# Optimization experiments

Measured on AMD Instinct MI355X. Metric: run time of the kernel, lower is better.

The kernel has to match this reference:

```python
import jax, jax.numpy as jnp
import numpy as np

TAU = 2.0      # LIF membrane time constant (spikingjelly default-style, decay_input=True)
VTH = 0.5      # v_threshold from init
S = 4          # time_steps
EPS = 1e-5     # BatchNorm eps
ALPHA = 4.0    # surrogate sigmoid alpha (spikingjelly Sigmoid default)

@jax.custom_vjp
def spike(x):
    # Heaviside forward (spikingjelly: x >= 0 -> 1)
    return (x >= 0.0).astype(x.dtype)

def _spike_fwd(x):
    return spike(x), x

def _spike_bwd(x, g):
    sg = jax.nn.sigmoid(ALPHA * x)
    return (g * ALPHA * sg * (1.0 - sg),)

spike.defvjp(_spike_fwd, _spike_bwd)

def bn(y, gamma, beta, mean, var):
    # inference-mode BatchNorm2d over channel axis 1; y: (B, C, T, V)
    inv = gamma * jax.lax.rsqrt(var + EPS)
    return y * inv[None, :, None, None] + (beta - mean * inv)[None, :, None, None]


def setup_inputs() -> dict:
    key = jax.random.key(0)
    ks = jax.random.split(key, 16)
    B, T, C, V, H, NC = 16, 512, 3, 16, 128, 12
    inp = {
        "x": jax.random.normal(ks[0], (B, T, C, V), dtype=jnp.float32),
        "w1": jax.random.normal(ks[1], (H, C), dtype=jnp.float32) * (1.0 / np.sqrt(C)),
        "b1": jax.random.normal(ks[2], (H,), dtype=jnp.float32) * 0.01,
        "g1": jnp.ones((H,), jnp.float32),
        "be1": jnp.zeros((H,), jnp.float32),
        "m1": jax.random.normal(ks[3], (H,), dtype=jnp.float32) * 0.1,
        "rv1": jax.random.uniform(ks[4], (H,), dtype=jnp.float32) + 0.5,
        "w2": jax.random.normal(ks[5], (H, H), dtype=jnp.float32) * (1.0 / np.sqrt(H)),
        "b2": jax.random.normal(ks[6], (H,), dtype=jnp.float32) * 0.01,
        "g2": jnp.ones((H,), jnp.float32),
        "be2": jnp.zeros((H,), jnp.float32),
        "m2": jax.random.normal(ks[7], (H,), dtype=jnp.float32) * 0.1,
        "rv2": jax.random.uniform(ks[8], (H,), dtype=jnp.float32) + 0.5,
        "wc": jax.random.normal(ks[9], (NC, H), dtype=jnp.float32) * (1.0 / np.sqrt(H)),
        "bc": jax.random.normal(ks[10], (NC,), dtype=jnp.float32) * 0.01,
    }
    return inp


def reference(x, w1, b1, g1, be1, m1, rv1, w2, b2, g2, be2, m2, rv2, wc, bc):
    # x: (B, T, C, V) -> channels-first (B, C, T, V) as in torch permute
    xc = jnp.transpose(x, (0, 2, 1, 3))
    # fc1 1x1 conv + BN; input identical across all S steps, so compute once
    h1 = bn(jnp.einsum('bctv,oc->botv', xc, w1) + b1[None, :, None, None],
            g1, be1, m1, rv1)  # (B, H, T, V)

    def step(carry, _):
        v1s, v2s, acc = carry
        # LIF1: decay_input=True, v_reset=0 hard reset
        v1n = v1s + (h1 - v1s) / TAU
        s1 = spike(v1n - VTH)
        v1n = v1n * (1.0 - s1)
        # fc2 1x1 conv + BN on spikes
        h2 = bn(jnp.einsum('botv,po->bptv', s1, w2) + b2[None, :, None, None],
                g2, be2, m2, rv2)
        # LIF2
        v2n = v2s + (h2 - v2s) / TAU
        s2 = spike(v2n - VTH)
        v2n = v2n * (1.0 - s2)
        return (v1n, v2n, acc + s2), None

    z = jnp.zeros_like(h1)
    (_, _, acc), _ = jax.lax.scan(step, (z, z, z), None, length=S)
    # mean over S, then mean over T and V -> (B, H); dropout is identity in eval
    feat = (acc / S).mean(axis=(2, 3))
    return feat @ wc.T + bc
```

## Files before the change

kernel.cpp:

```cpp
#include <hip/hip_runtime.h>
#include <hip/hip_bf16.h>
#include <stdint.h>
#include <math.h>

#define B_ 16
#define T_ 512
#define V_ 16
#define H_ 128
#define NC_ 12

typedef float v2f __attribute__((ext_vector_type(2)));
typedef __attribute__((ext_vector_type(8))) short s8frag;
typedef __attribute__((ext_vector_type(16))) float f16frag;
typedef unsigned long long u64;


__device__ __forceinline__ unsigned short bf16_rne(float w) {
    unsigned u = __float_as_uint(w);
    unsigned r = (u + 0x7FFFu + ((u >> 16) & 1u)) >> 16;
    return (unsigned short)r;
}
__device__ __forceinline__ float bf16_f32(unsigned short h) {
    return __uint_as_float((unsigned)h << 16);
}
__device__ __forceinline__ void split8(const float* __restrict__ s, s8frag& hi, s8frag& lo) {
    #pragma unroll
    for (int j = 0; j < 8; ++j) {
        float w = s[j];
        unsigned short hb = bf16_rne(w);
        unsigned short lb = bf16_rne(w - bf16_f32(hb));
        hi[j] = (short)hb;
        lo[j] = (short)lb;
    }
}
__device__ __forceinline__ uint4 expand8(unsigned bt) {
    uint4 r;
    r.x = ((bt      & 1u) * 0x3F80u) | (((bt >> 1) & 1u) * 0x3F800000u);
    r.y = (((bt >> 2) & 1u) * 0x3F80u) | (((bt >> 3) & 1u) * 0x3F800000u);
    r.z = (((bt >> 4) & 1u) * 0x3F80u) | (((bt >> 5) & 1u) * 0x3F800000u);
    r.w = (((bt >> 6) & 1u) * 0x3F80u) | (((bt >> 7) & 1u) * 0x3F800000u);
    return r;
}

#define ROUNDS 8
__global__ __launch_bounds__(256, 3) void snn_main(
    const float* __restrict__ x,
    const float* __restrict__ w1, const float* __restrict__ b1,
    const float* __restrict__ g1, const float* __restrict__ be1,
    const float* __restrict__ m1, const float* __restrict__ rv1,
    const float* __restrict__ w2, const float* __restrict__ b2,
    const float* __restrict__ g2, const float* __restrict__ be2,
    const float* __restrict__ m2, const float* __restrict__ rv2,
    float* __restrict__ feat)
{
    __shared__ uint4 afrag[2][2][8][64];
    __shared__ uint4 msk[4][16];
    __shared__ float xs[8 * 3 * V_];

    const int tid  = threadIdx.x;
    const int lane = tid & 63;
    const int wv   = tid >> 6;
    const int nl   = lane & 15;
    const int kg   = (lane >> 4) & 1;
    const int ch4  = lane >> 5;
    const int bb   = blockIdx.x >> 6;
    const int sbase = (blockIdx.x & 63) * (ROUNDS * 16);

    if (tid < 96) {
        const float4* xb = (const float4*)(x + ((size_t)(bb * T_ + (sbase >> 4)) * 3) * V_);
        ((float4*)xs)[tid] = xb[tid];
    }

    const int p = lane, q = lane + 64;
    v2f w0v = { w1[p*3+0], w1[q*3+0] };
    v2f w1v = { w1[p*3+1], w1[q*3+1] };
    v2f w2v = { w1[p*3+2], w1[q*3+2] };
    v2f b1v = { b1[p], b1[q] };
    float i1a = g1[p] * (float)(1.0 / sqrt((double)(rv1[p] + 1e-5f)));
    float i1b = g1[q] * (float)(1.0 / sqrt((double)(rv1[q] + 1e-5f)));
    v2f i1v = { i1a, i1b };
    v2f d1v = { be1[p] - m1[p] * i1a, be1[q] - m1[q] * i1b };

    const int chn = wv * 32 + (lane & 31);
    float i2c = g2[chn] * (float)(1.0 / sqrt((double)(rv2[chn] + 1e-5f)));
    float d2c = be2[chn] - m2[chn] * i2c;
    float b2c = b2[chn];

    s8frag bh[8], bl[8];
    #pragma unroll
    for (int c = 0; c < 8; ++c)
        split8(&w2[chn * H_ + c * 16 + ch4 * 8], bh[c], bl[c]);

    __syncthreads();

    float facc = 0.f;

    #define CONSUME(BUF)                                                        \
        {                                                                       \
            f16frag acc0 = {0.f,0.f,0.f,0.f,0.f,0.f,0.f,0.f,                    \
                            0.f,0.f,0.f,0.f,0.f,0.f,0.f,0.f};                   \
            f16frag acc1 = acc0;                                                \
            _Pragma("unroll")                                                   \
            for (int c = 0; c < 8; ++c) {                                       \
                s8frag a0 = *(const s8frag*)&afrag[BUF][0][c][lane];            \
                s8frag a1 = *(const s8frag*)&afrag[BUF][1][c][lane];            \
                acc0 = __builtin_amdgcn_mfma_f32_32x32x16_bf16(a0, bh[c], acc0, 0,0,0); \
                acc1 = __builtin_amdgcn_mfma_f32_32x32x16_bf16(a1, bh[c], acc1, 0,0,0); \
                acc0 = __builtin_amdgcn_mfma_f32_32x32x16_bf16(a0, bl[c], acc0, 0,0,0); \
                acc1 = __builtin_amdgcn_mfma_f32_32x32x16_bf16(a1, bl[c], acc1, 0,0,0); \
            }                                                                   \
            _Pragma("unroll")                                                   \
            for (int tt = 0; tt < 2; ++tt) {                                    \
                const f16frag accs = tt ? acc1 : acc0;                          \
                _Pragma("unroll")                                               \
                for (int g = 0; g < 4; ++g) {                                   \
                    float v = 0.f;                                              \
                    _Pragma("unroll")                                           \
                    for (int s = 0; s < 4; ++s) {                               \
                        float h2 = (accs[g*4+s] + b2c) * i2c + d2c;             \
                        v = v + (h2 - v) * 0.5f;                                \
                        bool sp = v >= 0.5f;                                    \
                        v = sp ? 0.f : v;                                       \
                        facc += sp ? 1.f : 0.f;                                 \
                    }                                                           \
                }                                                               \
            }                                                                   \
        }

    for (int r = 0; r < ROUNDS; ++r) {
        #pragma unroll
        for (int i = 0; i < 4; ++i) {
            int ls = r * 16 + wv * 4 + i;
            int tl = ls >> 4, v = ls & 15;
            const float* xp = &xs[tl * 48 + v];
            float x0 = xp[0], x1 = xp[V_], x2 = xp[2 * V_];

            v2f h1 = ((x0 * w0v + x1 * w1v + x2 * w2v) + b1v) * i1v + d1v;
            v2f v1t = h1 * 0.5f;
            v2f v2t = v1t + h1 * 0.25f;
            v2f v3t = v2t + (h1 - v2t) * 0.5f;
            v2f v4t = v3t + (h1 - v3t) * 0.5f;

            u64 t1a = __ballot(v1t.x >= 0.5f), t2a = __ballot(v2t.x >= 0.5f);
            u64 t3a = __ballot(v3t.x >= 0.5f), t4a = __ballot(v4t.x >= 0.5f);
            u64 t1b = __ballot(v1t.y >= 0.5f), t2b = __ballot(v2t.y >= 0.5f);
            u64 t3b = __ballot(v3t.y >= 0.5f), t4b = __ballot(v4t.y >= 0.5f);
            u64 s3a = t1a | (t3a & ~t2a), s3b = t1b | (t3b & ~t2b);
            u64 s4a = t2a | (t4a & ~t3a), s4b = t2b | (t4b & ~t3b);

            u64 mx = (lane == 0) ? t1a : (lane == 1) ? t2a : (lane == 2) ? s3a : s4a;
            u64 my = (lane == 0) ? t1b : (lane == 1) ? t2b : (lane == 2) ? s3b : s4b;
            if (lane < 4) {
                uint4 mm;
                mm.x = (unsigned)mx; mm.y = (unsigned)(mx >> 32);
                mm.z = (unsigned)my; mm.w = (unsigned)(my >> 32);
                msk[wv][i * 4 + lane] = mm;
            }
        }
        {
            uint4 mm = msk[wv][nl];
            u64 wsel = ch4 ? ((u64)mm.z | ((u64)mm.w << 32))
                           : ((u64)mm.x | ((u64)mm.y << 32));
            int tt   = wv >> 1;
            int slot = ((wv & 1) * 16 + nl) + 32 * kg;
            int buf  = r & 1;
            #pragma unroll
            for (int j = 0; j < 4; ++j) {
                unsigned by = (unsigned)(wsel >> (kg * 8 + j * 16)) & 0xFFu;
                afrag[buf][tt][ch4 * 4 + j][slot] = expand8(by);
            }
        }
        if (r > 0) { int pb = (r - 1) & 1; CONSUME(pb); }
        __syncthreads();
    }
    { int pb = (ROUNDS - 1) & 1; CONSUME(pb); }
    #undef CONSUME

    facc += __shfl_xor(facc, 32);
    if (lane < 32) atomicAdd(&feat[bb * H_ + chn], facc);
}

__global__ __launch_bounds__(128) void classifier_kernel(
    const float* __restrict__ feat,
    const float* __restrict__ wc,
    const float* __restrict__ bc,
    float* __restrict__ out) {
    __shared__ float fb[H_];
    int b = blockIdx.x, t = threadIdx.x;
    fb[t] = feat[b * H_ + t] * (1.0f / 32768.0f);
    __syncthreads();
    if (t < NC_) {
        float s = 0.f;
        for (int h = 0; h < H_; ++h) s += fb[h] * wc[t * H_ + h];
        out[b * NC_ + t] = s + bc[t];
    }
}

extern "C" void kernel_launch(void* const* d_in, const int* in_sizes, int n_in,
                              void* d_out, int out_size, void* d_ws, size_t ws_size,
                              hipStream_t stream) {
    const float* x   = (const float*)d_in[0];
    const float* w1  = (const float*)d_in[1];
    const float* b1  = (const float*)d_in[2];
    const float* g1  = (const float*)d_in[3];
    const float* be1 = (const float*)d_in[4];
    const float* m1  = (const float*)d_in[5];
    const float* rv1 = (const float*)d_in[6];
    const float* m2  = (const float*)d_in[11];
    const float* w2  = (const float*)d_in[7];
    const float* b2  = (const float*)d_in[8];
    const float* g2  = (const float*)d_in[9];
    const float* be2 = (const float*)d_in[10];
    const float* rv2 = (const float*)d_in[12];
    const float* wc  = (const float*)d_in[13];
    const float* bc  = (const float*)d_in[14];

    float* feat = (float*)d_ws;
    float* out  = (float*)d_out;

    snn_main<<<1024, 256, 0, stream>>>(x, w1, b1, g1, be1, m1, rv1,
                                       w2, b2, g2, be2, m2, rv2, feat);
    classifier_kernel<<<B_, 128, 0, stream>>>(feat, wc, bc, out);
}
```

Measured before the change: 137.3 us.

## Halve rounds per block, drop double buffer, raise occupancy and MFMA priority

Each block now handles half as many rounds, so the grid doubles, and the launch-bound occupancy hint goes from 3 to 6 blocks per CU. The double-buffered afrag staging becomes a single buffer. The software pipeline, where the MFMA for the previous round overlapped with building spikes for the current one, is replaced by a straight sequence: build, sync, MFMA under raised s_setprio, sync, then LIF2. The bias is folded into one fmaf. The intent is to hide latency through more resident waves rather than intra-block pipelining, at the cost of an extra barrier per round and more per-block setup, including the w2 bf16 split repeated by twice as many blocks.

```diff
diff --git a/kernel.cpp b/kernel.cpp
--- a/kernel.cpp
+++ b/kernel.cpp
@@ -42,8 +42,8 @@
     return r;
 }
 
-#define ROUNDS 8
-__global__ __launch_bounds__(256, 3) void snn_main(
+#define ROUNDS 4
+__global__ __launch_bounds__(256, 6) void snn_main(
     const float* __restrict__ x,
     const float* __restrict__ w1, const float* __restrict__ b1,
     const float* __restrict__ g1, const float* __restrict__ be1,
@@ -53,9 +53,9 @@
     const float* __restrict__ m2, const float* __restrict__ rv2,
     float* __restrict__ feat)
 {
-    __shared__ uint4 afrag[2][2][8][64];
+    __shared__ uint4 afrag[2][8][64];
     __shared__ uint4 msk[4][16];
-    __shared__ float xs[8 * 3 * V_];
+    __shared__ float xs[ROUNDS * 2 * 3 * V_];
 
     const int tid  = threadIdx.x;
     const int lane = tid & 63;
@@ -63,10 +63,10 @@
     const int nl   = lane & 15;
     const int kg   = (lane >> 4) & 1;
     const int ch4  = lane >> 5;
-    const int bb   = blockIdx.x >> 6;
-    const int sbase = (blockIdx.x & 63) * (ROUNDS * 16);
-
-    if (tid < 96) {
+    const int bb   = blockIdx.x >> 7;
+    const int sbase = (blockIdx.x & 127) * (ROUNDS * 16);
+
+    if (tid < 48) {
         const float4* xb = (const float4*)(x + ((size_t)(bb * T_ + (sbase >> 4)) * 3) * V_);
         ((float4*)xs)[tid] = xb[tid];
     }
@@ -84,7 +84,7 @@
     const int chn = wv * 32 + (lane & 31);
     float i2c = g2[chn] * (float)(1.0 / sqrt((double)(rv2[chn] + 1e-5f)));
     float d2c = be2[chn] - m2[chn] * i2c;
-    float b2c = b2[chn];
+    float dd2 = fmaf(b2[chn], i2c, d2c);
 
     s8frag bh[8], bl[8];
     #pragma unroll
@@ -94,38 +94,7 @@
     __syncthreads();
 
     float facc = 0.f;
-
-    #define CONSUME(BUF)                                                        \
-        {                                                                       \
-            f16frag acc0 = {0.f,0.f,0.f,0.f,0.f,0.f,0.f,0.f,                    \
-                            0.f,0.f,0.f,0.f,0.f,0.f,0.f,0.f};                   \
-            f16frag acc1 = acc0;                                                \
-            _Pragma("unroll")                                                   \
-            for (int c = 0; c < 8; ++c) {                                       \
-                s8frag a0 = *(const s8frag*)&afrag[BUF][0][c][lane];            \
-                s8frag a1 = *(const s8frag*)&afrag[BUF][1][c][lane];            \
-                acc0 = __builtin_amdgcn_mfma_f32_32x32x16_bf16(a0, bh[c], acc0, 0,0,0); \
-                acc1 = __builtin_amdgcn_mfma_f32_32x32x16_bf16(a1, bh[c], acc1, 0,0,0); \
-                acc0 = __builtin_amdgcn_mfma_f32_32x32x16_bf16(a0, bl[c], acc0, 0,0,0); \
-                acc1 = __builtin_amdgcn_mfma_f32_32x32x16_bf16(a1, bl[c], acc1, 0,0,0); \
-            }                                                                   \
-            _Pragma("unroll")                                                   \
-            for (int tt = 0; tt < 2; ++tt) {                                    \
-                const f16frag accs = tt ? acc1 : acc0;                          \
-                _Pragma("unroll")                                               \
-                for (int g = 0; g < 4; ++g) {                                   \
-                    float v = 0.f;                                              \
-                    _Pragma("unroll")                                           \
-                    for (int s = 0; s < 4; ++s) {                               \
-                        float h2 = (accs[g*4+s] + b2c) * i2c + d2c;             \
-                        v = v + (h2 - v) * 0.5f;                                \
-                        bool sp = v >= 0.5f;                                    \
-                        v = sp ? 0.f : v;                                       \
-                        facc += sp ? 1.f : 0.f;                                 \
-                    }                                                           \
-                }                                                               \
-            }                                                                   \
-        }
+    f16frag acc0, acc1;
 
     for (int r = 0; r < ROUNDS; ++r) {
         #pragma unroll
@@ -163,18 +132,47 @@
                            : ((u64)mm.x | ((u64)mm.y << 32));
             int tt   = wv >> 1;
             int slot = ((wv & 1) * 16 + nl) + 32 * kg;
-            int buf  = r & 1;
             #pragma unroll
             for (int j = 0; j < 4; ++j) {
                 unsigned by = (unsigned)(wsel >> (kg * 8 + j * 16)) & 0xFFu;
-                afrag[buf][tt][ch4 * 4 + j][slot] = expand8(by);
+                afrag[tt][ch4 * 4 + j][slot] = expand8(by);
             }
         }
-        if (r > 0) { int pb = (r - 1) & 1; CONSUME(pb); }
         __syncthreads();
-    }
-    { int pb = (ROUNDS - 1) & 1; CONSUME(pb); }
-    #undef CONSUME
+
+        acc0 = (f16frag){0.f,0.f,0.f,0.f,0.f,0.f,0.f,0.f,
+                         0.f,0.f,0.f,0.f,0.f,0.f,0.f,0.f};
+        acc1 = acc0;
+        __builtin_amdgcn_s_setprio(1);
+        #pragma unroll
+        for (int c = 0; c < 8; ++c) {
+            s8frag a0 = *(const s8frag*)&afrag[0][c][lane];
+            s8frag a1 = *(const s8frag*)&afrag[1][c][lane];
+            acc0 = __builtin_amdgcn_mfma_f32_32x32x16_bf16(a0, bh[c], acc0, 0,0,0);
+            acc1 = __builtin_amdgcn_mfma_f32_32x32x16_bf16(a1, bh[c], acc1, 0,0,0);
+            acc0 = __builtin_amdgcn_mfma_f32_32x32x16_bf16(a0, bl[c], acc0, 0,0,0);
+            acc1 = __builtin_amdgcn_mfma_f32_32x32x16_bf16(a1, bl[c], acc1, 0,0,0);
+        }
+        __builtin_amdgcn_s_setprio(0);
+        if (r + 1 < ROUNDS) __syncthreads();
+
+        #pragma unroll
+        for (int tt = 0; tt < 2; ++tt) {
+            const f16frag accs = tt ? acc1 : acc0;
+            #pragma unroll
+            for (int g = 0; g < 4; ++g) {
+                float v = 0.f;
+                #pragma unroll
+                for (int s = 0; s < 4; ++s) {
+                    float h2 = fmaf(accs[g*4+s], i2c, dd2);
+                    v = v + (h2 - v) * 0.5f;
+                    bool sp = v >= 0.5f;
+                    v = sp ? 0.f : v;
+                    facc += sp ? 1.f : 0.f;
+                }
+            }
+        }
+    }
 
     facc += __shfl_xor(facc, 32);
     if (lane < 32) atomicAdd(&feat[bb * H_ + chn], facc);
@@ -206,11 +204,11 @@
     const float* be1 = (const float*)d_in[4];
     const float* m1  = (const float*)d_in[5];
     const float* rv1 = (const float*)d_in[6];
-    const float* m2  = (const float*)d_in[11];
     const float* w2  = (const float*)d_in[7];
     const float* b2  = (const float*)d_in[8];
     const float* g2  = (const float*)d_in[9];
     const float* be2 = (const float*)d_in[10];
+    const float* m2  = (const float*)d_in[11];
     const float* rv2 = (const float*)d_in[12];
     const float* wc  = (const float*)d_in[13];
     const float* bc  = (const float*)d_in[14];
@@ -218,7 +216,7 @@
     float* feat = (float*)d_ws;
     float* out  = (float*)d_out;
 
-    snn_main<<<1024, 256, 0, stream>>>(x, w1, b1, g1, be1, m1, rv1,
+    snn_main<<<2048, 256, 0, stream>>>(x, w1, b1, g1, be1, m1, rv1,
                                        w2, b2, g2, be2, m2, rv2, feat);
     classifier_kernel<<<B_, 128, 0, stream>>>(feat, wc, bc, out);
 }
```

After: 183.0 us. 1.33x slower.

## Warp-specialize SNN kernel into producer and MFMA consumer waves

Applied to the files above, without the earlier changes.

Splits each 512-thread block into four producer waves, which compute fc1, LIF1 and the expanded spike fragments, and four consumer waves, which run the bf16 MFMA fc2 plus LIF2. The two roles ping-pong through a double-buffered LDS area, so spike generation overlaps the matrix work. Blocks now cover twice as many positions, and MFMA sections are wrapped in s_setprio. The bias and BN terms fold into one fma. The aim is to hide the ALU/ballot producer latency behind the MFMA work, at the cost of each wave holding only half the register state and fewer, larger blocks.

```diff
diff --git a/kernel.cpp b/kernel.cpp
--- a/kernel.cpp
+++ b/kernel.cpp
@@ -13,6 +13,7 @@
 typedef __attribute__((ext_vector_type(8))) short s8frag;
 typedef __attribute__((ext_vector_type(16))) float f16frag;
 typedef unsigned long long u64;
+
 
 
 __device__ __forceinline__ unsigned short bf16_rne(float w) {
@@ -42,8 +43,8 @@
     return r;
 }
 
-#define ROUNDS 8
-__global__ __launch_bounds__(256, 3) void snn_main(
+#define NSR 8
+__global__ __launch_bounds__(512, 2) void snn_main(
     const float* __restrict__ x,
     const float* __restrict__ w1, const float* __restrict__ b1,
     const float* __restrict__ g1, const float* __restrict__ be1,
@@ -53,131 +54,148 @@
     const float* __restrict__ m2, const float* __restrict__ rv2,
     float* __restrict__ feat)
 {
-    __shared__ uint4 afrag[2][2][8][64];
-    __shared__ uint4 msk[4][16];
-    __shared__ float xs[8 * 3 * V_];
+    __shared__ uint4 afrag[2][4][8][64];
+    __shared__ uint4 msk[4][32];
+    __shared__ float xs[16 * 3 * V_];
 
     const int tid  = threadIdx.x;
     const int lane = tid & 63;
     const int wv   = tid >> 6;
-    const int nl   = lane & 15;
-    const int kg   = (lane >> 4) & 1;
-    const int ch4  = lane >> 5;
-    const int bb   = blockIdx.x >> 6;
-    const int sbase = (blockIdx.x & 63) * (ROUNDS * 16);
-
-    if (tid < 96) {
+    const bool producer = (wv < 4);
+    const int rw   = wv & 3;
+    const int row  = lane & 31;
+    const int half = lane >> 5;
+    const int bb   = blockIdx.x >> 5;
+    const int sbase = (blockIdx.x & 31) * (NSR * 32);
+
+    if (tid < 192) {
         const float4* xb = (const float4*)(x + ((size_t)(bb * T_ + (sbase >> 4)) * 3) * V_);
         ((float4*)xs)[tid] = xb[tid];
     }
 
-    const int p = lane, q = lane + 64;
-    v2f w0v = { w1[p*3+0], w1[q*3+0] };
-    v2f w1v = { w1[p*3+1], w1[q*3+1] };
-    v2f w2v = { w1[p*3+2], w1[q*3+2] };
-    v2f b1v = { b1[p], b1[q] };
-    float i1a = g1[p] * (float)(1.0 / sqrt((double)(rv1[p] + 1e-5f)));
-    float i1b = g1[q] * (float)(1.0 / sqrt((double)(rv1[q] + 1e-5f)));
-    v2f i1v = { i1a, i1b };
-    v2f d1v = { be1[p] - m1[p] * i1a, be1[q] - m1[q] * i1b };
-
-    const int chn = wv * 32 + (lane & 31);
-    float i2c = g2[chn] * (float)(1.0 / sqrt((double)(rv2[chn] + 1e-5f)));
-    float d2c = be2[chn] - m2[chn] * i2c;
-    float b2c = b2[chn];
-
+    v2f w0v, w1v, w2v, b1v, i1v, d1v;
     s8frag bh[8], bl[8];
-    #pragma unroll
-    for (int c = 0; c < 8; ++c)
-        split8(&w2[chn * H_ + c * 16 + ch4 * 8], bh[c], bl[c]);
+    float i2c = 0.f, dd2 = 0.f;
+    int chn = 0;
+    if (producer) {
+        const int p = lane, q = lane + 64;
+        w0v = (v2f){ w1[p*3+0], w1[q*3+0] };
+        w1v = (v2f){ w1[p*3+1], w1[q*3+1] };
+        w2v = (v2f){ w1[p*3+2], w1[q*3+2] };
+        b1v = (v2f){ b1[p], b1[q] };
+        float i1a = g1[p] * (float)(1.0 / sqrt((double)(rv1[p] + 1e-5f)));
+        float i1b = g1[q] * (float)(1.0 / sqrt((double)(rv1[q] + 1e-5f)));
+        i1v = (v2f){ i1a, i1b };
+        d1v = (v2f){ be1[p] - m1[p] * i1a, be1[q] - m1[q] * i1b };
+    } else {
+        chn = rw * 32 + (lane & 31);
+        i2c = g2[chn] * (float)(1.0 / sqrt((double)(rv2[chn] + 1e-5f)));
+        float d2c = be2[chn] - m2[chn] * i2c;
+        dd2 = fmaf(b2[chn], i2c, d2c);
+        #pragma unroll
+        for (int c = 0; c < 8; ++c)
+            split8(&w2[chn * H_ + c * 16 + half * 8], bh[c], bl[c]);
+    }
 
     __syncthreads();
 
     float facc = 0.f;
+
+    #define BUILD_EXPAND(SR, BUF)                                               \
+        {                                                                       \
+            _Pragma("unroll")                                                   \
+            for (int i = 0; i < 8; ++i) {                                       \
+                int ls = (SR) * 32 + rw * 8 + i;         \
+                int tl = ls >> 4, v = ls & 15;                                  \
+                const float* xp = &xs[tl * 48 + v];                             \
+                float x0 = xp[0], x1 = xp[V_], x2 = xp[2 * V_];                 \
+                v2f h1 = ((x0 * w0v + x1 * w1v + x2 * w2v) + b1v) * i1v + d1v;  \
+                v2f v1t = h1 * 0.5f;                                            \
+                v2f v2t = v1t + h1 * 0.25f;                                     \
+                v2f v3t = v2t + (h1 - v2t) * 0.5f;                              \
+                v2f v4t = v3t + (h1 - v3t) * 0.5f;                              \
+                u64 t1a = __ballot(v1t.x >= 0.5f), t2a = __ballot(v2t.x >= 0.5f);\
+                u64 t3a = __ballot(v3t.x >= 0.5f), t4a = __ballot(v4t.x >= 0.5f);\
+                u64 t1b = __ballot(v1t.y >= 0.5f), t2b = __ballot(v2t.y >= 0.5f);\
+                u64 t3b = __ballot(v3t.y >= 0.5f), t4b = __ballot(v4t.y >= 0.5f);\
+                u64 s3a = t1a | (t3a & ~t2a), s3b = t1b | (t3b & ~t2b);         \
+                u64 s4a = t2a | (t4a & ~t3a), s4b = t2b | (t4b & ~t3b);         \
+                u64 mx = (lane == 0) ? t1a : (lane == 1) ? t2a : (lane == 2) ? s3a : s4a; \
+                u64 my = (lane == 0) ? t1b : (lane == 1) ? t2b : (lane == 2) ? s3b : s4b; \
+                if (lane < 4) {                                                 \
+                    uint4 mm;                                                   \
+                    mm.x = (unsigned)mx; mm.y = (unsigned)(mx >> 32);           \
+                    mm.z = (unsigned)my; mm.w = (unsigned)(my >> 32);           \
+                    msk[rw][i * 4 + lane] = mm;                                 \
+                }                                                               \
+            }                                                                   \
+            uint4 mm = msk[rw][row];               \
+            u64 wsel = half ? ((u64)mm.z | ((u64)mm.w << 32))                   \
+                            : ((u64)mm.x | ((u64)mm.y << 32));                  \
+            _Pragma("unroll")                                                   \
+            for (int kg = 0; kg < 2; ++kg)                                      \
+                _Pragma("unroll")                                               \
+                for (int j = 0; j < 4; ++j) {                                   \
+                    unsigned by = (unsigned)(wsel >> (kg * 8 + j * 16)) & 0xFFu;\
+                    afrag[BUF][rw][half * 4 + j][row + 32 * kg] = expand8(by);  \
+                }                                                               \
+        }
 
     #define CONSUME(BUF)                                                        \
         {                                                                       \
-            f16frag acc0 = {0.f,0.f,0.f,0.f,0.f,0.f,0.f,0.f,                    \
-                            0.f,0.f,0.f,0.f,0.f,0.f,0.f,0.f};                   \
-            f16frag acc1 = acc0;                                                \
             _Pragma("unroll")                                                   \
-            for (int c = 0; c < 8; ++c) {                                       \
-                s8frag a0 = *(const s8frag*)&afrag[BUF][0][c][lane];            \
-                s8frag a1 = *(const s8frag*)&afrag[BUF][1][c][lane];            \
-                acc0 = __builtin_amdgcn_mfma_f32_32x32x16_bf16(a0, bh[c], acc0, 0,0,0); \
-                acc1 = __builtin_amdgcn_mfma_f32_32x32x16_bf16(a1, bh[c], acc1, 0,0,0); \
-                acc0 = __builtin_amdgcn_mfma_f32_32x32x16_bf16(a0, bl[c], acc0, 0,0,0); \
-                acc1 = __builtin_amdgcn_mfma_f32_32x32x16_bf16(a1, bl[c], acc1, 0,0,0); \
-            }                                                                   \
-            _Pragma("unroll")                                                   \
-            for (int tt = 0; tt < 2; ++tt) {                                    \
-                const f16frag accs = tt ? acc1 : acc0;                          \
+            for (int tp = 0; tp < 2; ++tp) {                                    \
+                f16frag acc0 = {0.f,0.f,0.f,0.f,0.f,0.f,0.f,0.f,                \
+                                0.f,0.f,0.f,0.f,0.f,0.f,0.f,0.f};               \
+                f16frag acc1 = acc0;                                            \
+                __builtin_amdgcn_s_setprio(1);                                  \
                 _Pragma("unroll")                                               \
-                for (int g = 0; g < 4; ++g) {                                   \
-                    float v = 0.f;                                              \
+                for (int c = 0; c < 8; ++c) {                                   \
+                    s8frag a0 = *(const s8frag*)&afrag[BUF][tp * 2][c][lane];   \
+                    s8frag a1 = *(const s8frag*)&afrag[BUF][tp * 2 + 1][c][lane];\
+                    acc0 = __builtin_amdgcn_mfma_f32_32x32x16_bf16(a0, bh[c], acc0, 0,0,0); \
+                    acc1 = __builtin_amdgcn_mfma_f32_32x32x16_bf16(a1, bh[c], acc1, 0,0,0); \
+                    acc0 = __builtin_amdgcn_mfma_f32_32x32x16_bf16(a0, bl[c], acc0, 0,0,0); \
+                    acc1 = __builtin_amdgcn_mfma_f32_32x32x16_bf16(a1, bl[c], acc1, 0,0,0); \
+                }                                                               \
+                __builtin_amdgcn_s_setprio(0);                                  \
+                _Pragma("unroll")                                               \
+                for (int tt = 0; tt < 2; ++tt) {                                \
+                    const f16frag accs = tt ? acc1 : acc0;                      \
                     _Pragma("unroll")                                           \
-                    for (int s = 0; s < 4; ++s) {                               \
-                        float h2 = (accs[g*4+s] + b2c) * i2c + d2c;             \
-                        v = v + (h2 - v) * 0.5f;                                \
-                        bool sp = v >= 0.5f;                                    \
-                        v = sp ? 0.f : v;                                       \
-                        facc += sp ? 1.f : 0.f;                                 \
+                    for (int g = 0; g < 4; ++g) {                               \
+                        float v = 0.f;                                          \
+                        _Pragma("unroll")                                       \
+                        for (int s = 0; s < 4; ++s) {                           \
+                            float h2 = fmaf(accs[g*4+s], i2c, dd2);             \
+                            v = v + (h2 - v) * 0.5f;                            \
+                            bool sp = v >= 0.5f;                                \
+                            v = sp ? 0.f : v;                                   \
+                            facc += sp ? 1.f : 0.f;                             \
+                        }                                                       \
                     }                                                           \
                 }                                                               \
             }                                                                   \
         }
 
-    for (int r = 0; r < ROUNDS; ++r) {
-        #pragma unroll
-        for (int i = 0; i < 4; ++i) {
-            int ls = r * 16 + wv * 4 + i;
-            int tl = ls >> 4, v = ls & 15;
-            const float* xp = &xs[tl * 48 + v];
-            float x0 = xp[0], x1 = xp[V_], x2 = xp[2 * V_];
-
-            v2f h1 = ((x0 * w0v + x1 * w1v + x2 * w2v) + b1v) * i1v + d1v;
-            v2f v1t = h1 * 0.5f;
-            v2f v2t = v1t + h1 * 0.25f;
-            v2f v3t = v2t + (h1 - v2t) * 0.5f;
-            v2f v4t = v3t + (h1 - v3t) * 0.5f;
-
-            u64 t1a = __ballot(v1t.x >= 0.5f), t2a = __ballot(v2t.x >= 0.5f);
-            u64 t3a = __ballot(v3t.x >= 0.5f), t4a = __ballot(v4t.x >= 0.5f);
-            u64 t1b = __ballot(v1t.y >= 0.5f), t2b = __ballot(v2t.y >= 0.5f);
-            u64 t3b = __ballot(v3t.y >= 0.5f), t4b = __ballot(v4t.y >= 0.5f);
-            u64 s3a = t1a | (t3a & ~t2a), s3b = t1b | (t3b & ~t2b);
-            u64 s4a = t2a | (t4a & ~t3a), s4b = t2b | (t4b & ~t3b);
-
-            u64 mx = (lane == 0) ? t1a : (lane == 1) ? t2a : (lane == 2) ? s3a : s4a;
-            u64 my = (lane == 0) ? t1b : (lane == 1) ? t2b : (lane == 2) ? s3b : s4b;
-            if (lane < 4) {
-                uint4 mm;
-                mm.x = (unsigned)mx; mm.y = (unsigned)(mx >> 32);
-                mm.z = (unsigned)my; mm.w = (unsigned)(my >> 32);
-                msk[wv][i * 4 + lane] = mm;
-            }
+    if (producer) BUILD_EXPAND(0, 0);
+    __syncthreads();
+    for (int sr = 0; sr < NSR; ++sr) {
+        int cur = sr & 1;
+        if (producer) {
+            if (sr + 1 < NSR) BUILD_EXPAND(sr + 1, cur ^ 1);
+        } else {
+            CONSUME(cur);
         }
-        {
-            uint4 mm = msk[wv][nl];
-            u64 wsel = ch4 ? ((u64)mm.z | ((u64)mm.w << 32))
-                           : ((u64)mm.x | ((u64)mm.y << 32));
-            int tt   = wv >> 1;
-            int slot = ((wv & 1) * 16 + nl) + 32 * kg;
-            int buf  = r & 1;
-            #pragma unroll
-            for (int j = 0; j < 4; ++j) {
-                unsigned by = (unsigned)(wsel >> (kg * 8 + j * 16)) & 0xFFu;
-                afrag[buf][tt][ch4 * 4 + j][slot] = expand8(by);
-            }
-        }
-        if (r > 0) { int pb = (r - 1) & 1; CONSUME(pb); }
         __syncthreads();
     }
-    { int pb = (ROUNDS - 1) & 1; CONSUME(pb); }
+    #undef BUILD_EXPAND
     #undef CONSUME
 
-    facc += __shfl_xor(facc, 32);
-    if (lane < 32) atomicAdd(&feat[bb * H_ + chn], facc);
+    if (!producer) {
+        facc += __shfl_xor(facc, 32);
+        if (lane < 32) atomicAdd(&feat[bb * H_ + chn], facc);
+    }
 }
 
 __global__ __launch_bounds__(128) void classifier_kernel(
@@ -206,11 +224,11 @@
     const float* be1 = (const float*)d_in[4];
     const float* m1  = (const float*)d_in[5];
     const float* rv1 = (const float*)d_in[6];
-    const float* m2  = (const float*)d_in[11];
     const float* w2  = (const float*)d_in[7];
     const float* b2  = (const float*)d_in[8];
     const float* g2  = (const float*)d_in[9];
     const float* be2 = (const float*)d_in[10];
+    const float* m2  = (const float*)d_in[11];
     const float* rv2 = (const float*)d_in[12];
     const float* wc  = (const float*)d_in[13];
     const float* bc  = (const float*)d_in[14];
@@ -218,7 +236,7 @@
     float* feat = (float*)d_ws;
     float* out  = (float*)d_out;
 
-    snn_main<<<1024, 256, 0, stream>>>(x, w1, b1, g1, be1, m1, rv1,
-                                       w2, b2, g2, be2, m2, rv2, feat);
+    snn_main<<<512, 512, 0, stream>>>(x, w1, b1, g1, be1, m1, rv1,
+                                      w2, b2, g2, be2, m2, rv2, feat);
     classifier_kernel<<<B_, 128, 0, stream>>>(feat, wc, bc, out);
 }
```

New measurement: 138.8 us. No clear change (+1.0%).
